# Optimization experiments

Measured on AMD Instinct MI355X. Metric: run time of the kernel, lower is better.

## Reference

```python
import jax, jax.numpy as jnp
import numpy as np

N_NODES = 50000
N_EDGES = 800000
N_GRAPHS = 64
F_IN, F_HID, F_OUT = 128, 128, 16


def _graph_conv(x, W, b, src, dst, activation=None):
    """DGL GraphConv with norm='both': D_out^{-1/2} A^T D_in^{-1/2} X W + b."""
    n = x.shape[0]
    ones = jnp.ones((src.shape[0],), dtype=x.dtype)
    deg_out = jnp.clip(jax.ops.segment_sum(ones, src, num_segments=n), 1.0)
    deg_in = jnp.clip(jax.ops.segment_sum(ones, dst, num_segments=n), 1.0)
    h = x * jax.lax.rsqrt(deg_out)[:, None]          # scale by src out-degree
    agg = jax.ops.segment_sum(h[src], dst, num_segments=n)  # gather+scatter-add
    agg = agg * jax.lax.rsqrt(deg_in)[:, None]       # scale by dst in-degree
    out = agg @ W + b
    if activation is not None:
        out = activation(out)
    return out


def setup_inputs() -> dict:
    key = jax.random.key(0)
    ks = jax.random.split(key, 6)
    x = jax.random.normal(ks[0], (N_NODES, F_IN), dtype=jnp.float32)
    W1 = jax.random.normal(ks[1], (F_IN, F_HID), dtype=jnp.float32) * (F_IN ** -0.5)
    b1 = jnp.zeros((F_HID,), dtype=jnp.float32)
    W2 = jax.random.normal(ks[2], (F_HID, F_OUT), dtype=jnp.float32) * (F_HID ** -0.5)
    b2 = jnp.zeros((F_OUT,), dtype=jnp.float32)
    src = jax.random.randint(ks[3], (N_EDGES,), 0, N_NODES, dtype=jnp.int32)
    dst = jax.random.randint(ks[4], (N_EDGES,), 0, N_NODES, dtype=jnp.int32)
    graph_ids = jnp.sort(jax.random.randint(ks[5], (N_NODES,), 0, N_GRAPHS, dtype=jnp.int32))
    return {"x": x, "W1": W1, "b1": b1, "W2": W2, "b2": b2,
            "src": src, "dst": dst, "graph_ids": graph_ids}


def reference(x, W1, b1, W2, b2, src, dst, graph_ids):
    h = _graph_conv(x, W1, b1, src, dst, activation=jax.nn.relu)
    h = _graph_conv(h, W2, b2, src, dst, activation=None)
    # dgl.mean_nodes: per-graph mean over nodes
    sums = jax.ops.segment_sum(h, graph_ids, num_segments=N_GRAPHS)
    counts = jnp.clip(jax.ops.segment_sum(jnp.ones((N_NODES,), h.dtype), graph_ids,
                                          num_segments=N_GRAPHS), 1.0)
    return sums / counts[:, None]
```

## Files before the change

kernel.cpp:

```cpp
#include <hip/hip_runtime.h>
#include <hip/hip_bf16.h>

#define N_NODES_C 50000
#define N_EDGES_C 800000
#define N_GRAPHS_C 64
#define NBKT 782
#define BKTP 784
#define CHUNK 4096
#define NBLK_E 196

typedef __attribute__((ext_vector_type(8))) short bf16x8;
typedef __attribute__((ext_vector_type(4))) float f32x4;

__device__ __forceinline__ unsigned short f2bf(float f) {
    unsigned u = __float_as_uint(f);
    unsigned r = (u + 0x7FFFu + ((u >> 16) & 1u)) >> 16;
    return (unsigned short)r;
}

__global__ __launch_bounds__(256) void k_hist(
    const int* __restrict__ src, const int* __restrict__ dst,
    int* __restrict__ hmatD, int* __restrict__ hmatS, int nE)
{
    __shared__ int hD[BKTP], hS[BKTP];
    const int tid = threadIdx.x, blk = blockIdx.x;
    for (int i = tid; i < BKTP; i += 256) { hD[i] = 0; hS[i] = 0; }
    __syncthreads();
    const int base = blk * CHUNK;
    for (int i = tid; i < CHUNK; i += 256) {
        int e = base + i;
        if (e < nE) {
            atomicAdd(&hD[dst[e] >> 6], 1);
            atomicAdd(&hS[src[e] >> 6], 1);
        }
    }
    __syncthreads();
    for (int i = tid; i < BKTP; i += 256) {
        hmatD[blk * BKTP + i] = hD[i];
        hmatS[blk * BKTP + i] = hS[i];
    }
}

__global__ __launch_bounds__(64) void k_btot(
    const int* __restrict__ hmatD, const int* __restrict__ hmatS,
    int* __restrict__ btotD, int* __restrict__ btotS)
{
    const int b = blockIdx.x, lane = threadIdx.x;
    const int* hm = blockIdx.y ? hmatS : hmatD;
    int v = 0;
    for (int blk = lane; blk < NBLK_E; blk += 64) v += hm[blk * BKTP + b];
#pragma unroll
    for (int off = 32; off > 0; off >>= 1) v += __shfl_down(v, off, 64);
    if (lane == 0) (blockIdx.y ? btotS : btotD)[b] = v;
}

__global__ __launch_bounds__(1024) void k_bscan(
    const int* __restrict__ btotD, const int* __restrict__ btotS,
    int* __restrict__ bbaseD, int* __restrict__ bbaseS)
{
    __shared__ int part[1024];
    const int tid = threadIdx.x;
    const int* bt = blockIdx.x ? btotS : btotD;
    int* bb = blockIdx.x ? bbaseS : bbaseD;
    int v = (tid < NBKT) ? bt[tid] : 0;
    part[tid] = v;
    __syncthreads();
    for (int off = 1; off < 1024; off <<= 1) {
        int t = (tid >= off) ? part[tid - off] : 0;
        __syncthreads();
        part[tid] += t;
        __syncthreads();
    }
    if (tid < NBKT) bb[tid] = part[tid] - v;
    if (tid == NBKT - 1) bb[NBKT] = part[tid];
}

__global__ __launch_bounds__(256) void k_boff(
    const int* __restrict__ hmatD, const int* __restrict__ hmatS,
    const int* __restrict__ bbaseD, const int* __restrict__ bbaseS,
    int* __restrict__ offmatD, int* __restrict__ offmatS)
{
    __shared__ int part[256];
    const int b = blockIdx.x, tid = threadIdx.x;
    const int* hm = blockIdx.y ? hmatS : hmatD;
    const int* bb = blockIdx.y ? bbaseS : bbaseD;
    int* om = blockIdx.y ? offmatS : offmatD;
    int v = (tid < NBLK_E) ? hm[tid * BKTP + b] : 0;
    part[tid] = v;
    __syncthreads();
    for (int off = 1; off < 256; off <<= 1) {
        int t = (tid >= off) ? part[tid - off] : 0;
        __syncthreads();
        part[tid] += t;
        __syncthreads();
    }
    if (tid < NBLK_E) om[tid * BKTP + b] = bb[b] + part[tid] - v;
}

__global__ __launch_bounds__(256) void k_scat(
    const int* __restrict__ src, const int* __restrict__ dst,
    const int* __restrict__ offmatD, const int* __restrict__ offmatS,
    unsigned* __restrict__ ed, unsigned char* __restrict__ es, int nE)
{
    __shared__ int curD[BKTP], curS[BKTP];
    const int tid = threadIdx.x, blk = blockIdx.x;
    for (int i = tid; i < BKTP; i += 256) {
        curD[i] = offmatD[blk * BKTP + i];
        curS[i] = offmatS[blk * BKTP + i];
    }
    __syncthreads();
    const int base = blk * CHUNK;
    for (int i = tid; i < CHUNK; i += 256) {
        int e = base + i;
        if (e < nE) {
            unsigned s = (unsigned)src[e], d = (unsigned)dst[e];
            int pD = atomicAdd(&curD[d >> 6], 1);
            ed[pD] = (d << 16) | s;
            int pS = atomicAdd(&curS[s >> 6], 1);
            es[pS] = (unsigned char)(s & 63u);
        }
    }
}

__global__ __launch_bounds__(256) void k_bucket(
    const unsigned* __restrict__ ed, const unsigned char* __restrict__ es,
    const int* __restrict__ bbaseD, const int* __restrict__ bbaseS,
    int* __restrict__ rowptr, float* __restrict__ rsI, float* __restrict__ rsO,
    unsigned short* __restrict__ csr_src, int nV)
{
    __shared__ int cnt[64], cur[64];
    const int tid = threadIdx.x;
    const int side = (blockIdx.x >= NBKT);
    const int b = side ? blockIdx.x - NBKT : blockIdx.x;

    if (tid < 64) cnt[tid] = 0;
    __syncthreads();

    if (!side) {
        const int lo = bbaseD[b], hi = bbaseD[b + 1];
        for (int j = lo + tid; j < hi; j += 256)
            atomicAdd(&cnt[(ed[j] >> 16) & 63u], 1);
        __syncthreads();
        if (tid < 64) {
            int c = cnt[tid];
            int v = c;
#pragma unroll
            for (int off = 1; off < 64; off <<= 1) {
                int n = __shfl_up(v, off, 64);
                if (tid >= off) v += n;
            }
            int excl = v - c;
            int node = b * 64 + tid;
            if (node <= nV) rowptr[node] = lo + excl;
            if (node < nV) rsI[node] = rsqrtf((float)max(c, 1));
            cur[tid] = excl;
        }
        __syncthreads();
        for (int j = lo + tid; j < hi; j += 256) {
            unsigned v = ed[j];
            int p = atomicAdd(&cur[(v >> 16) & 63u], 1);
            csr_src[lo + p] = (unsigned short)(v & 0xFFFFu);
        }
    } else {
        const int lo = bbaseS[b], hi = bbaseS[b + 1];
        for (int j = lo + tid; j < hi; j += 256)
            atomicAdd(&cnt[es[j]], 1);
        __syncthreads();
        if (tid < 64) {
            int node = b * 64 + tid;
            if (node < nV) rsO[node] = rsqrtf((float)max(cnt[tid], 1));
        }
    }
}

__global__ __launch_bounds__(256) void k_prep(
    const float* __restrict__ x, const float* __restrict__ rsO,
    unsigned short* __restrict__ xs, int nV)
{
    int t = blockIdx.x * 256 + threadIdx.x;
    if (t >= nV * 32) return;
    int v = t >> 5, q = t & 31;
    float w = rsO[v];
    float4 a = ((const float4*)(x + (size_t)v * 128))[q];
    ushort4 o;
    o.x = f2bf(a.x * w); o.y = f2bf(a.y * w);
    o.z = f2bf(a.z * w); o.w = f2bf(a.w * w);
    ((ushort4*)(xs + (size_t)v * 128))[q] = o;
}

__global__ __launch_bounds__(256) void k_wconv(
    const float* __restrict__ W1, const float* __restrict__ W2,
    unsigned short* __restrict__ w1f, unsigned short* __restrict__ w2f)
{
    int t = blockIdx.x * 256 + threadIdx.x;
    if (t < 2048) {
        int kk = t >> 9, nt = (t >> 6) & 7, l = t & 63;
        int kb = kk * 32 + ((l >> 4) << 3), n = nt * 16 + (l & 15);
        ushort4 lo, hi;
        lo.x = f2bf(W1[(kb + 0) * 128 + n]); lo.y = f2bf(W1[(kb + 1) * 128 + n]);
        lo.z = f2bf(W1[(kb + 2) * 128 + n]); lo.w = f2bf(W1[(kb + 3) * 128 + n]);
        hi.x = f2bf(W1[(kb + 4) * 128 + n]); hi.y = f2bf(W1[(kb + 5) * 128 + n]);
        hi.z = f2bf(W1[(kb + 6) * 128 + n]); hi.w = f2bf(W1[(kb + 7) * 128 + n]);
        ((ushort4*)(w1f + t * 8))[0] = lo;
        ((ushort4*)(w1f + t * 8))[1] = hi;
    } else if (t < 2304) {
        int t2 = t - 2048;
        int kk = t2 >> 6, l = t2 & 63;
        int kb = kk * 32 + ((l >> 4) << 3), n = l & 15;
        ushort4 lo, hi;
        lo.x = f2bf(W2[(kb + 0) * 16 + n]); lo.y = f2bf(W2[(kb + 1) * 16 + n]);
        lo.z = f2bf(W2[(kb + 2) * 16 + n]); lo.w = f2bf(W2[(kb + 3) * 16 + n]);
        hi.x = f2bf(W2[(kb + 4) * 16 + n]); hi.y = f2bf(W2[(kb + 5) * 16 + n]);
        hi.z = f2bf(W2[(kb + 6) * 16 + n]); hi.w = f2bf(W2[(kb + 7) * 16 + n]);
        ((ushort4*)(w2f + t2 * 8))[0] = lo;
        ((ushort4*)(w2f + t2 * 8))[1] = hi;
    }
}

__global__ __launch_bounds__(256) void k_agg1b(
    const unsigned short* __restrict__ xs, const int* __restrict__ rowptr,
    const unsigned short* __restrict__ csr_src, const float* __restrict__ rsI,
    unsigned short* __restrict__ agg1b, int nV)
{
    long long t = (long long)blockIdx.x * blockDim.x + threadIdx.x;
    int v = (int)(t >> 6);
    int lane = (int)(t & 63);
    if (v >= nV) return;
    int g = lane >> 4, fl = lane & 15;
    int beg = rowptr[v], end = rowptr[v + 1];
    float acc[8];
#pragma unroll
    for (int k = 0; k < 8; ++k) acc[k] = 0.f;

    for (int j = beg + g; j < end; j += 4) {
        int s = csr_src[j];
        uint4 w = *(const uint4*)(xs + (size_t)s * 128 + fl * 8);
        acc[0] += __uint_as_float(w.x << 16);
        acc[1] += __uint_as_float(w.x & 0xFFFF0000u);
        acc[2] += __uint_as_float(w.y << 16);
        acc[3] += __uint_as_float(w.y & 0xFFFF0000u);
        acc[4] += __uint_as_float(w.z << 16);
        acc[5] += __uint_as_float(w.z & 0xFFFF0000u);
        acc[6] += __uint_as_float(w.w << 16);
        acc[7] += __uint_as_float(w.w & 0xFFFF0000u);
    }
#pragma unroll
    for (int k = 0; k < 8; ++k) {
        acc[k] += __shfl_xor(acc[k], 16, 64);
        acc[k] += __shfl_xor(acc[k], 32, 64);
    }
    float ri = rsI[v];
    if (g < 2) {
        ushort4 o;
        o.x = f2bf(acc[g * 4 + 0] * ri);
        o.y = f2bf(acc[g * 4 + 1] * ri);
        o.z = f2bf(acc[g * 4 + 2] * ri);
        o.w = f2bf(acc[g * 4 + 3] * ri);
        *(ushort4*)(agg1b + (size_t)v * 128 + fl * 8 + g * 4) = o;
    }
}

__global__ __launch_bounds__(256) void k_mfma(
    const unsigned short* __restrict__ agg1b, const float* __restrict__ b1,
    const unsigned short* __restrict__ w1f, const unsigned short* __restrict__ w2f,
    const float* __restrict__ rsO, unsigned short* __restrict__ y, int nV)
{
    __shared__ __align__(16) unsigned short h1[64 * 136];
    const int tid = threadIdx.x;
    const int w = tid >> 6, l = tid & 63;
    const int lr = l & 15, lg = l >> 4;
    const int row0 = blockIdx.x * 64;

    bf16x8 a[4];
    const unsigned short* abase = agg1b + (size_t)(row0 + w * 16 + lr) * 128 + lg * 8;
#pragma unroll
    for (int kk = 0; kk < 4; ++kk)
        a[kk] = *(const bf16x8*)(abase + kk * 32);

    f32x4 acc[8];
#pragma unroll
    for (int nt = 0; nt < 8; ++nt) acc[nt] = (f32x4){0.f, 0.f, 0.f, 0.f};

#pragma unroll
    for (int nt = 0; nt < 8; ++nt)
#pragma unroll
        for (int kk = 0; kk < 4; ++kk) {
            bf16x8 b = *(const bf16x8*)(w1f + ((kk * 8 + nt) * 64 + l) * 8);
            acc[nt] = __builtin_amdgcn_mfma_f32_16x16x32_bf16(a[kk], b, acc[nt], 0, 0, 0);
        }

#pragma unroll
    for (int nt = 0; nt < 8; ++nt) {
        float bb = b1[nt * 16 + lr];
#pragma unroll
        for (int i = 0; i < 4; ++i) {
            float h = fmaxf(acc[nt][i] + bb, 0.f);
            h1[(w * 16 + lg * 4 + i) * 136 + nt * 16 + lr] = f2bf(h);
        }
    }
    __syncthreads();

    f32x4 acc2 = (f32x4){0.f, 0.f, 0.f, 0.f};
#pragma unroll
    for (int kk = 0; kk < 4; ++kk) {
        bf16x8 a2 = *(const bf16x8*)(&h1[(w * 16 + lr) * 136 + kk * 32 + lg * 8]);
        bf16x8 b2 = *(const bf16x8*)(w2f + (kk * 64 + l) * 8);
        acc2 = __builtin_amdgcn_mfma_f32_16x16x32_bf16(a2, b2, acc2, 0, 0, 0);
    }
#pragma unroll
    for (int i = 0; i < 4; ++i) {
        int r = row0 + w * 16 + lg * 4 + i;
        if (r < nV) y[(size_t)r * 16 + lr] = f2bf(acc2[i] * rsO[r]);
    }
}

__global__ __launch_bounds__(256) void k_agg2(
    const unsigned short* __restrict__ y, const int* __restrict__ rowptr,
    const unsigned short* __restrict__ csr_src, float* __restrict__ agg2, int nV)
{
    long long t = (long long)blockIdx.x * blockDim.x + threadIdx.x;
    int v = (int)(t >> 6);
    int lane = (int)(t & 63);
    if (v >= nV) return;
    int f = lane & 15, g = lane >> 4;
    int beg = rowptr[v], end = rowptr[v + 1];
    float acc = 0.f;
    for (int j = beg + g; j < end; j += 4) {
        int s = csr_src[j];
        unsigned u = y[(size_t)s * 16 + f];
        acc += __uint_as_float(u << 16);
    }
    acc += __shfl_xor(acc, 16, 64);
    acc += __shfl_xor(acc, 32, 64);
    if (g == 0) agg2[(size_t)v * 16 + f] = acc;
}

__device__ __forceinline__ int lowerb(const int* __restrict__ a, int n, int key) {
    int lo = 0, hi = n;
    while (lo < hi) { int m = (lo + hi) >> 1; if (a[m] < key) lo = m + 1; else hi = m; }
    return lo;
}

__global__ __launch_bounds__(256) void k_pool(
    const float* __restrict__ agg2, const float* __restrict__ rsI,
    const int* __restrict__ gid, const float* __restrict__ b2,
    float* __restrict__ out, int nV)
{
    __shared__ float red[256][16];
    const int g = blockIdx.x;
    const int tid = threadIdx.x;
    const int lo = lowerb(gid, nV, g);
    const int hi = lowerb(gid, nV, g + 1);

    float acc[16];
#pragma unroll
    for (int f = 0; f < 16; ++f) acc[f] = 0.f;

    for (int v = lo + tid; v < hi; v += 256) {
        float w = rsI[v];
        const float4* p = (const float4*)(agg2 + (size_t)v * 16);
        float4 a = p[0], b = p[1], c = p[2], d = p[3];
        acc[0] += a.x * w; acc[1] += a.y * w; acc[2]  += a.z * w; acc[3]  += a.w * w;
        acc[4] += b.x * w; acc[5] += b.y * w; acc[6]  += b.z * w; acc[7]  += b.w * w;
        acc[8] += c.x * w; acc[9] += c.y * w; acc[10] += c.z * w; acc[11] += c.w * w;
        acc[12] += d.x * w; acc[13] += d.y * w; acc[14] += d.z * w; acc[15] += d.w * w;
    }
#pragma unroll
    for (int f = 0; f < 16; ++f) red[tid][f] = acc[f];
    __syncthreads();
    for (int s = 128; s > 0; s >>= 1) {
        if (tid < s)
#pragma unroll
            for (int f = 0; f < 16; ++f) red[tid][f] += red[tid + s][f];
        __syncthreads();
    }
    if (tid < 16) {
        int n = hi - lo;
        out[g * 16 + tid] = (n > 0) ? (red[0][tid] / (float)n + b2[tid]) : 0.f;
    }
}

extern "C" void kernel_launch(void* const* d_in, const int* in_sizes, int n_in,
                              void* d_out, int out_size, void* d_ws, size_t ws_size,
                              hipStream_t stream) {
    const float* x   = (const float*)d_in[0];
    const float* W1  = (const float*)d_in[1];
    const float* b1  = (const float*)d_in[2];
    const float* W2  = (const float*)d_in[3];
    const float* b2  = (const float*)d_in[4];
    const int*   src = (const int*)d_in[5];
    const int*   dst = (const int*)d_in[6];
    const int*   gid = (const int*)d_in[7];
    float* out = (float*)d_out;

    int* p = (int*)d_ws;
    int*   btotD   = p;            p += 784;
    int*   btotS   = p;            p += 784;
    int*   bbaseD  = p;            p += 800;
    int*   bbaseS  = p;            p += 800;
    int*   rowptr  = p;            p += 50432;
    float* rsO     = (float*)p;    p += 50176;
    float* rsI     = (float*)p;    p += 50176;
    unsigned short* csr_src = (unsigned short*)p; p += 400128;
    unsigned short* w1f = (unsigned short*)p;     p += 8192;
    unsigned short* w2f = (unsigned short*)p;     p += 1024;
    unsigned short* y   = (unsigned short*)p;     p += 401408;
    float* agg2    = (float*)p;    p += 800000;
    int*   BIG     = p;
    int*   hmatD   = BIG;
    int*   hmatS   = BIG + 153664;
    int*   offmatD = BIG + 307328;
    int*   offmatS = BIG + 460992;
    unsigned*      ed = (unsigned*)(BIG + 614656);
    unsigned char* es = (unsigned char*)(BIG + 1414656);
    unsigned short* xs    = (unsigned short*)BIG;
    unsigned short* agg1b = (unsigned short*)(BIG + 3211264);

    k_hist <<<NBLK_E, 256, 0, stream>>>(src, dst, hmatD, hmatS, N_EDGES_C);
    k_btot <<<dim3(NBKT, 2), 64, 0, stream>>>(hmatD, hmatS, btotD, btotS);
    k_bscan<<<2, 1024, 0, stream>>>(btotD, btotS, bbaseD, bbaseS);
    k_boff <<<dim3(NBKT, 2), 256, 0, stream>>>(hmatD, hmatS, bbaseD, bbaseS, offmatD, offmatS);
    k_scat <<<NBLK_E, 256, 0, stream>>>(src, dst, offmatD, offmatS, ed, es, N_EDGES_C);
    k_bucket<<<2 * NBKT, 256, 0, stream>>>(ed, es, bbaseD, bbaseS, rowptr, rsI, rsO, csr_src, N_NODES_C);

    k_wconv<<<9, 256, 0, stream>>>(W1, W2, w1f, w2f);
    k_prep <<<(N_NODES_C * 32 + 255) / 256, 256, 0, stream>>>(x, rsO, xs, N_NODES_C);
    k_agg1b<<<(N_NODES_C * 64 + 255) / 256, 256, 0, stream>>>(xs, rowptr, csr_src, rsI, agg1b, N_NODES_C);
    k_mfma <<<(N_NODES_C + 63) / 64, 256, 0, stream>>>(agg1b, b1, w1f, w2f, rsO, y, N_NODES_C);
    k_agg2 <<<(N_NODES_C * 64 + 255) / 256, 256, 0, stream>>>(y, rowptr, csr_src, agg2, N_NODES_C);
    k_pool <<<N_GRAPHS_C, 256, 0, stream>>>(agg2, rsI, gid, b2, out, N_NODES_C);
}
```

Before: 132.3 us.

## Fuse bucket totals into scan, merge prep kernels, fuse agg2 with pooling

Folds the per-bucket total reduction into the scan kernel, merges the x-scaling and weight-conversion kernels into one launch, and unrolls the layer-1 gather loop by two to keep more loads in flight. The layer-2 aggregation now accumulates directly into per-graph sums in shared memory and flushes them to a global buffer with atomics, so the agg2 intermediate and the separate pooling kernel go away. The intent is fewer launches and less global traffic. In exchange the scan serialises 196 loads per thread, and float atomics make the summation order nondeterministic.

```diff
diff --git a/kernel.cpp b/kernel.cpp
--- a/kernel.cpp
+++ b/kernel.cpp
@@ -41,28 +41,19 @@
     }
 }
 
-__global__ __launch_bounds__(64) void k_btot(
+__global__ __launch_bounds__(1024) void k_bscan(
     const int* __restrict__ hmatD, const int* __restrict__ hmatS,
-    int* __restrict__ btotD, int* __restrict__ btotS)
-{
-    const int b = blockIdx.x, lane = threadIdx.x;
-    const int* hm = blockIdx.y ? hmatS : hmatD;
-    int v = 0;
-    for (int blk = lane; blk < NBLK_E; blk += 64) v += hm[blk * BKTP + b];
-#pragma unroll
-    for (int off = 32; off > 0; off >>= 1) v += __shfl_down(v, off, 64);
-    if (lane == 0) (blockIdx.y ? btotS : btotD)[b] = v;
-}
-
-__global__ __launch_bounds__(1024) void k_bscan(
-    const int* __restrict__ btotD, const int* __restrict__ btotS,
-    int* __restrict__ bbaseD, int* __restrict__ bbaseS)
+    int* __restrict__ bbaseD, int* __restrict__ bbaseS,
+    float* __restrict__ accbuf)
 {
     __shared__ int part[1024];
     const int tid = threadIdx.x;
-    const int* bt = blockIdx.x ? btotS : btotD;
+    const int* hm = blockIdx.x ? hmatS : hmatD;
     int* bb = blockIdx.x ? bbaseS : bbaseD;
-    int v = (tid < NBKT) ? bt[tid] : 0;
+    if (blockIdx.x == 0) accbuf[tid] = 0.f;
+    int v = 0;
+    if (tid < NBKT)
+        for (int blk = 0; blk < NBLK_E; ++blk) v += hm[blk * BKTP + tid];
     part[tid] = v;
     __syncthreads();
     for (int off = 1; off < 1024; off <<= 1) {
@@ -173,26 +164,26 @@
     }
 }
 
-__global__ __launch_bounds__(256) void k_prep(
+__global__ __launch_bounds__(256) void k_prepw(
     const float* __restrict__ x, const float* __restrict__ rsO,
-    unsigned short* __restrict__ xs, int nV)
-{
-    int t = blockIdx.x * 256 + threadIdx.x;
-    if (t >= nV * 32) return;
-    int v = t >> 5, q = t & 31;
-    float w = rsO[v];
-    float4 a = ((const float4*)(x + (size_t)v * 128))[q];
-    ushort4 o;
-    o.x = f2bf(a.x * w); o.y = f2bf(a.y * w);
-    o.z = f2bf(a.z * w); o.w = f2bf(a.w * w);
-    ((ushort4*)(xs + (size_t)v * 128))[q] = o;
-}
-
-__global__ __launch_bounds__(256) void k_wconv(
     const float* __restrict__ W1, const float* __restrict__ W2,
-    unsigned short* __restrict__ w1f, unsigned short* __restrict__ w2f)
-{
-    int t = blockIdx.x * 256 + threadIdx.x;
+    unsigned short* __restrict__ xs, unsigned short* __restrict__ w1f,
+    unsigned short* __restrict__ w2f, int nV)
+{
+    const int tid = threadIdx.x;
+    if (blockIdx.x < 6250) {
+        int t = blockIdx.x * 256 + tid;
+        if (t >= nV * 32) return;
+        int v = t >> 5, q = t & 31;
+        float w = rsO[v];
+        float4 a = ((const float4*)(x + (size_t)v * 128))[q];
+        ushort4 o;
+        o.x = f2bf(a.x * w); o.y = f2bf(a.y * w);
+        o.z = f2bf(a.z * w); o.w = f2bf(a.w * w);
+        ((ushort4*)(xs + (size_t)v * 128))[q] = o;
+        return;
+    }
+    int t = (blockIdx.x - 6250) * 256 + tid;
     if (t < 2048) {
         int kk = t >> 9, nt = (t >> 6) & 7, l = t & 63;
         int kb = kk * 32 + ((l >> 4) << 3), n = nt * 16 + (l & 15);
@@ -232,7 +223,30 @@
 #pragma unroll
     for (int k = 0; k < 8; ++k) acc[k] = 0.f;
 
-    for (int j = beg + g; j < end; j += 4) {
+    int j = beg + g;
+    while (j + 4 < end) {
+        int s0 = csr_src[j], s1 = csr_src[j + 4];
+        uint4 w0 = *(const uint4*)(xs + (size_t)s0 * 128 + fl * 8);
+        uint4 w1 = *(const uint4*)(xs + (size_t)s1 * 128 + fl * 8);
+        acc[0] += __uint_as_float(w0.x << 16);
+        acc[1] += __uint_as_float(w0.x & 0xFFFF0000u);
+        acc[2] += __uint_as_float(w0.y << 16);
+        acc[3] += __uint_as_float(w0.y & 0xFFFF0000u);
+        acc[4] += __uint_as_float(w0.z << 16);
+        acc[5] += __uint_as_float(w0.z & 0xFFFF0000u);
+        acc[6] += __uint_as_float(w0.w << 16);
+        acc[7] += __uint_as_float(w0.w & 0xFFFF0000u);
+        acc[0] += __uint_as_float(w1.x << 16);
+        acc[1] += __uint_as_float(w1.x & 0xFFFF0000u);
+        acc[2] += __uint_as_float(w1.y << 16);
+        acc[3] += __uint_as_float(w1.y & 0xFFFF0000u);
+        acc[4] += __uint_as_float(w1.z << 16);
+        acc[5] += __uint_as_float(w1.z & 0xFFFF0000u);
+        acc[6] += __uint_as_float(w1.w << 16);
+        acc[7] += __uint_as_float(w1.w & 0xFFFF0000u);
+        j += 8;
+    }
+    if (j < end) {
         int s = csr_src[j];
         uint4 w = *(const uint4*)(xs + (size_t)s * 128 + fl * 8);
         acc[0] += __uint_as_float(w.x << 16);
@@ -314,25 +328,38 @@
     }
 }
 
-__global__ __launch_bounds__(256) void k_agg2(
+__global__ __launch_bounds__(256) void k_agg2p(
     const unsigned short* __restrict__ y, const int* __restrict__ rowptr,
-    const unsigned short* __restrict__ csr_src, float* __restrict__ agg2, int nV)
-{
-    long long t = (long long)blockIdx.x * blockDim.x + threadIdx.x;
-    int v = (int)(t >> 6);
-    int lane = (int)(t & 63);
-    if (v >= nV) return;
-    int f = lane & 15, g = lane >> 4;
-    int beg = rowptr[v], end = rowptr[v + 1];
-    float acc = 0.f;
-    for (int j = beg + g; j < end; j += 4) {
-        int s = csr_src[j];
-        unsigned u = y[(size_t)s * 16 + f];
-        acc += __uint_as_float(u << 16);
-    }
-    acc += __shfl_xor(acc, 16, 64);
-    acc += __shfl_xor(acc, 32, 64);
-    if (g == 0) agg2[(size_t)v * 16 + f] = acc;
+    const unsigned short* __restrict__ csr_src, const float* __restrict__ rsI,
+    const int* __restrict__ gid, float* __restrict__ accbuf, int nV, int nwaves)
+{
+    __shared__ float gacc[N_GRAPHS_C * 16];
+    const int tid = threadIdx.x;
+    for (int i = tid; i < N_GRAPHS_C * 16; i += 256) gacc[i] = 0.f;
+    __syncthreads();
+
+    const int lane = tid & 63, f = lane & 15, g4 = lane >> 4;
+    int wglob = blockIdx.x * 4 + (tid >> 6);
+    for (int v = wglob; v < nV; v += nwaves) {
+        int beg = rowptr[v], end = rowptr[v + 1];
+        float acc = 0.f;
+        for (int j = beg + g4; j < end; j += 4) {
+            int s = csr_src[j];
+            unsigned u = y[(size_t)s * 16 + f];
+            acc += __uint_as_float(u << 16);
+        }
+        acc += __shfl_xor(acc, 16, 64);
+        acc += __shfl_xor(acc, 32, 64);
+        if (g4 == 0) {
+            float val = acc * rsI[v];
+            atomicAdd(&gacc[gid[v] * 16 + f], val);
+        }
+    }
+    __syncthreads();
+    for (int i = tid; i < N_GRAPHS_C * 16; i += 256) {
+        float v = gacc[i];
+        if (v != 0.f) unsafeAtomicAdd(&accbuf[i], v);
+    }
 }
 
 __device__ __forceinline__ int lowerb(const int* __restrict__ a, int n, int key) {
@@ -341,42 +368,20 @@
     return lo;
 }
 
-__global__ __launch_bounds__(256) void k_pool(
-    const float* __restrict__ agg2, const float* __restrict__ rsI,
-    const int* __restrict__ gid, const float* __restrict__ b2,
-    float* __restrict__ out, int nV)
-{
-    __shared__ float red[256][16];
-    const int g = blockIdx.x;
-    const int tid = threadIdx.x;
-    const int lo = lowerb(gid, nV, g);
-    const int hi = lowerb(gid, nV, g + 1);
-
-    float acc[16];
-#pragma unroll
-    for (int f = 0; f < 16; ++f) acc[f] = 0.f;
-
-    for (int v = lo + tid; v < hi; v += 256) {
-        float w = rsI[v];
-        const float4* p = (const float4*)(agg2 + (size_t)v * 16);
-        float4 a = p[0], b = p[1], c = p[2], d = p[3];
-        acc[0] += a.x * w; acc[1] += a.y * w; acc[2]  += a.z * w; acc[3]  += a.w * w;
-        acc[4] += b.x * w; acc[5] += b.y * w; acc[6]  += b.z * w; acc[7]  += b.w * w;
-        acc[8] += c.x * w; acc[9] += c.y * w; acc[10] += c.z * w; acc[11] += c.w * w;
-        acc[12] += d.x * w; acc[13] += d.y * w; acc[14] += d.z * w; acc[15] += d.w * w;
-    }
-#pragma unroll
-    for (int f = 0; f < 16; ++f) red[tid][f] = acc[f];
-    __syncthreads();
-    for (int s = 128; s > 0; s >>= 1) {
-        if (tid < s)
-#pragma unroll
-            for (int f = 0; f < 16; ++f) red[tid][f] += red[tid + s][f];
-        __syncthreads();
-    }
-    if (tid < 16) {
-        int n = hi - lo;
-        out[g * 16 + tid] = (n > 0) ? (red[0][tid] / (float)n + b2[tid]) : 0.f;
+__global__ __launch_bounds__(256) void k_fin(
+    const float* __restrict__ accbuf, const int* __restrict__ gid,
+    const float* __restrict__ b2, float* __restrict__ out, int nV)
+{
+    int t = threadIdx.x;
+    int g = t >> 2, f0 = (t & 3) * 4;
+    int lo = lowerb(gid, nV, g);
+    int hi = lowerb(gid, nV, g + 1);
+    int n = hi - lo;
+    float inv = (n > 0) ? 1.f / (float)n : 0.f;
+#pragma unroll
+    for (int k = 0; k < 4; ++k) {
+        int f = f0 + k;
+        out[g * 16 + f] = (n > 0) ? accbuf[g * 16 + f] * inv + b2[f] : 0.f;
     }
 }
 
@@ -394,8 +399,6 @@
     float* out = (float*)d_out;
 
     int* p = (int*)d_ws;
-    int*   btotD   = p;            p += 784;
-    int*   btotS   = p;            p += 784;
     int*   bbaseD  = p;            p += 800;
     int*   bbaseS  = p;            p += 800;
     int*   rowptr  = p;            p += 50432;
@@ -405,7 +408,7 @@
     unsigned short* w1f = (unsigned short*)p;     p += 8192;
     unsigned short* w2f = (unsigned short*)p;     p += 1024;
     unsigned short* y   = (unsigned short*)p;     p += 401408;
-    float* agg2    = (float*)p;    p += 800000;
+    float* accbuf  = (float*)p;    p += 1024;
     int*   BIG     = p;
     int*   hmatD   = BIG;
     int*   hmatS   = BIG + 153664;
@@ -417,16 +420,14 @@
     unsigned short* agg1b = (unsigned short*)(BIG + 3211264);
 
     k_hist <<<NBLK_E, 256, 0, stream>>>(src, dst, hmatD, hmatS, N_EDGES_C);
-    k_btot <<<dim3(NBKT, 2), 64, 0, stream>>>(hmatD, hmatS, btotD, btotS);
-    k_bscan<<<2, 1024, 0, stream>>>(btotD, btotS, bbaseD, bbaseS);
+    k_bscan<<<2, 1024, 0, stream>>>(hmatD, hmatS, bbaseD, bbaseS, accbuf);
     k_boff <<<dim3(NBKT, 2), 256, 0, stream>>>(hmatD, hmatS, bbaseD, bbaseS, offmatD, offmatS);
     k_scat <<<NBLK_E, 256, 0, stream>>>(src, dst, offmatD, offmatS, ed, es, N_EDGES_C);
     k_bucket<<<2 * NBKT, 256, 0, stream>>>(ed, es, bbaseD, bbaseS, rowptr, rsI, rsO, csr_src, N_NODES_C);
 
-    k_wconv<<<9, 256, 0, stream>>>(W1, W2, w1f, w2f);
-    k_prep <<<(N_NODES_C * 32 + 255) / 256, 256, 0, stream>>>(x, rsO, xs, N_NODES_C);
+    k_prepw<<<6259, 256, 0, stream>>>(x, rsO, W1, W2, xs, w1f, w2f, N_NODES_C);
     k_agg1b<<<(N_NODES_C * 64 + 255) / 256, 256, 0, stream>>>(xs, rowptr, csr_src, rsI, agg1b, N_NODES_C);
     k_mfma <<<(N_NODES_C + 63) / 64, 256, 0, stream>>>(agg1b, b1, w1f, w2f, rsO, y, N_NODES_C);
-    k_agg2 <<<(N_NODES_C * 64 + 255) / 256, 256, 0, stream>>>(y, rowptr, csr_src, agg2, N_NODES_C);
-    k_pool <<<N_GRAPHS_C, 256, 0, stream>>>(agg2, rsI, gid, b2, out, N_NODES_C);
-}
+    k_agg2p<<<256, 256, 0, stream>>>(y, rowptr, csr_src, rsI, gid, accbuf, N_NODES_C, 1024);
+    k_fin  <<<1, 256, 0, stream>>>(accbuf, gid, b2, out, N_NODES_C);
+}
```

New measurement: 198.8 us. 1.5x slower.

## Merge bucket-total pass into scan, fuse weight convert with prep, unroll gather

Applied to the files above, without the earlier changes.

Removes the separate bucket-total kernel by having each thread of the two-block scan sum its bucket column across all edge chunks itself. Merges the weight conversion into the feature-prep kernel as extra tail blocks, which cuts two kernel launches overall. Also unrolls the layer-1 neighbour gather loop by two so two row loads are in flight per iteration. The serial 196-iteration column sum in only two blocks may be slower than the parallel reduction it replaces.

```diff
diff --git a/kernel.cpp b/kernel.cpp
--- a/kernel.cpp
+++ b/kernel.cpp
@@ -41,28 +41,17 @@
     }
 }
 
-__global__ __launch_bounds__(64) void k_btot(
+__global__ __launch_bounds__(1024) void k_bscan(
     const int* __restrict__ hmatD, const int* __restrict__ hmatS,
-    int* __restrict__ btotD, int* __restrict__ btotS)
-{
-    const int b = blockIdx.x, lane = threadIdx.x;
-    const int* hm = blockIdx.y ? hmatS : hmatD;
-    int v = 0;
-    for (int blk = lane; blk < NBLK_E; blk += 64) v += hm[blk * BKTP + b];
-#pragma unroll
-    for (int off = 32; off > 0; off >>= 1) v += __shfl_down(v, off, 64);
-    if (lane == 0) (blockIdx.y ? btotS : btotD)[b] = v;
-}
-
-__global__ __launch_bounds__(1024) void k_bscan(
-    const int* __restrict__ btotD, const int* __restrict__ btotS,
     int* __restrict__ bbaseD, int* __restrict__ bbaseS)
 {
     __shared__ int part[1024];
     const int tid = threadIdx.x;
-    const int* bt = blockIdx.x ? btotS : btotD;
+    const int* hm = blockIdx.x ? hmatS : hmatD;
     int* bb = blockIdx.x ? bbaseS : bbaseD;
-    int v = (tid < NBKT) ? bt[tid] : 0;
+    int v = 0;
+    if (tid < NBKT)
+        for (int blk = 0; blk < NBLK_E; ++blk) v += hm[blk * BKTP + tid];
     part[tid] = v;
     __syncthreads();
     for (int off = 1; off < 1024; off <<= 1) {
@@ -173,26 +162,26 @@
     }
 }
 
-__global__ __launch_bounds__(256) void k_prep(
+__global__ __launch_bounds__(256) void k_prepw(
     const float* __restrict__ x, const float* __restrict__ rsO,
-    unsigned short* __restrict__ xs, int nV)
-{
-    int t = blockIdx.x * 256 + threadIdx.x;
-    if (t >= nV * 32) return;
-    int v = t >> 5, q = t & 31;
-    float w = rsO[v];
-    float4 a = ((const float4*)(x + (size_t)v * 128))[q];
-    ushort4 o;
-    o.x = f2bf(a.x * w); o.y = f2bf(a.y * w);
-    o.z = f2bf(a.z * w); o.w = f2bf(a.w * w);
-    ((ushort4*)(xs + (size_t)v * 128))[q] = o;
-}
-
-__global__ __launch_bounds__(256) void k_wconv(
     const float* __restrict__ W1, const float* __restrict__ W2,
-    unsigned short* __restrict__ w1f, unsigned short* __restrict__ w2f)
-{
-    int t = blockIdx.x * 256 + threadIdx.x;
+    unsigned short* __restrict__ xs, unsigned short* __restrict__ w1f,
+    unsigned short* __restrict__ w2f, int nV)
+{
+    const int tid = threadIdx.x;
+    if (blockIdx.x < 6250) {
+        int t = blockIdx.x * 256 + tid;
+        if (t >= nV * 32) return;
+        int v = t >> 5, q = t & 31;
+        float w = rsO[v];
+        float4 a = ((const float4*)(x + (size_t)v * 128))[q];
+        ushort4 o;
+        o.x = f2bf(a.x * w); o.y = f2bf(a.y * w);
+        o.z = f2bf(a.z * w); o.w = f2bf(a.w * w);
+        ((ushort4*)(xs + (size_t)v * 128))[q] = o;
+        return;
+    }
+    int t = (blockIdx.x - 6250) * 256 + tid;
     if (t < 2048) {
         int kk = t >> 9, nt = (t >> 6) & 7, l = t & 63;
         int kb = kk * 32 + ((l >> 4) << 3), n = nt * 16 + (l & 15);
@@ -232,7 +221,30 @@
 #pragma unroll
     for (int k = 0; k < 8; ++k) acc[k] = 0.f;
 
-    for (int j = beg + g; j < end; j += 4) {
+    int j = beg + g;
+    while (j + 4 < end) {
+        int s0 = csr_src[j], s1 = csr_src[j + 4];
+        uint4 w0 = *(const uint4*)(xs + (size_t)s0 * 128 + fl * 8);
+        uint4 w1 = *(const uint4*)(xs + (size_t)s1 * 128 + fl * 8);
+        acc[0] += __uint_as_float(w0.x << 16);
+        acc[1] += __uint_as_float(w0.x & 0xFFFF0000u);
+        acc[2] += __uint_as_float(w0.y << 16);
+        acc[3] += __uint_as_float(w0.y & 0xFFFF0000u);
+        acc[4] += __uint_as_float(w0.z << 16);
+        acc[5] += __uint_as_float(w0.z & 0xFFFF0000u);
+        acc[6] += __uint_as_float(w0.w << 16);
+        acc[7] += __uint_as_float(w0.w & 0xFFFF0000u);
+        acc[0] += __uint_as_float(w1.x << 16);
+        acc[1] += __uint_as_float(w1.x & 0xFFFF0000u);
+        acc[2] += __uint_as_float(w1.y << 16);
+        acc[3] += __uint_as_float(w1.y & 0xFFFF0000u);
+        acc[4] += __uint_as_float(w1.z << 16);
+        acc[5] += __uint_as_float(w1.z & 0xFFFF0000u);
+        acc[6] += __uint_as_float(w1.w << 16);
+        acc[7] += __uint_as_float(w1.w & 0xFFFF0000u);
+        j += 8;
+    }
+    if (j < end) {
         int s = csr_src[j];
         uint4 w = *(const uint4*)(xs + (size_t)s * 128 + fl * 8);
         acc[0] += __uint_as_float(w.x << 16);
@@ -394,8 +406,6 @@
     float* out = (float*)d_out;
 
     int* p = (int*)d_ws;
-    int*   btotD   = p;            p += 784;
-    int*   btotS   = p;            p += 784;
     int*   bbaseD  = p;            p += 800;
     int*   bbaseS  = p;            p += 800;
     int*   rowptr  = p;            p += 50432;
@@ -417,14 +427,12 @@
     unsigned short* agg1b = (unsigned short*)(BIG + 3211264);
 
     k_hist <<<NBLK_E, 256, 0, stream>>>(src, dst, hmatD, hmatS, N_EDGES_C);
-    k_btot <<<dim3(NBKT, 2), 64, 0, stream>>>(hmatD, hmatS, btotD, btotS);
-    k_bscan<<<2, 1024, 0, stream>>>(btotD, btotS, bbaseD, bbaseS);
+    k_bscan<<<2, 1024, 0, stream>>>(hmatD, hmatS, bbaseD, bbaseS);
     k_boff <<<dim3(NBKT, 2), 256, 0, stream>>>(hmatD, hmatS, bbaseD, bbaseS, offmatD, offmatS);
     k_scat <<<NBLK_E, 256, 0, stream>>>(src, dst, offmatD, offmatS, ed, es, N_EDGES_C);
     k_bucket<<<2 * NBKT, 256, 0, stream>>>(ed, es, bbaseD, bbaseS, rowptr, rsI, rsO, csr_src, N_NODES_C);
 
-    k_wconv<<<9, 256, 0, stream>>>(W1, W2, w1f, w2f);
-    k_prep <<<(N_NODES_C * 32 + 255) / 256, 256, 0, stream>>>(x, rsO, xs, N_NODES_C);
+    k_prepw<<<6259, 256, 0, stream>>>(x, rsO, W1, W2, xs, w1f, w2f, N_NODES_C);
     k_agg1b<<<(N_NODES_C * 64 + 255) / 256, 256, 0, stream>>>(xs, rowptr, csr_src, rsI, agg1b, N_NODES_C);
     k_mfma <<<(N_NODES_C + 63) / 64, 256, 0, stream>>>(agg1b, b1, w1f, w2f, rsO, y, N_NODES_C);
     k_agg2 <<<(N_NODES_C * 64 + 255) / 256, 256, 0, stream>>>(y, rowptr, csr_src, agg2, N_NODES_C);
```

After: 129.0 us. 2.4% less time.
